# Kernel optimization log

Hardware: AMD Instinct MI355X
Metric: run time of the kernel (lower is better)

The kernel has to match this reference:

```python
import jax, jax.numpy as jnp
import numpy as np

TEMPERATURE = 1.0
NEG = -1e9
EPS = 1e-8


def setup_inputs() -> dict:
    key = jax.random.key(0)
    k1, k2, k3 = jax.random.split(key, 3)
    B, H = 524288, 32
    scores = jax.random.normal(k1, (B, H), dtype=jnp.float32)
    rankings = jax.random.randint(k2, (B, H), 0, 33, dtype=jnp.int32)
    mask = jax.random.randint(k3, (B, H), 0, 2, dtype=jnp.int32).astype(bool)
    return {"scores": scores, "rankings": rankings, "mask": mask}


def reference(scores, rankings, mask):
    B, H = scores.shape
    # effective validity: horse present AND has a ranking > 0 (top_k=None)
    m = mask & (rankings > 0)
    # masked, temperature-scaled scores; -1e9 entries underflow to exactly 0 in softmax
    s = jnp.where(m, scores / TEMPERATURE, NEG)
    p = jax.nn.softmax(s, axis=1)  # [B, H], ~0 at invalid slots

    n_valid = jnp.sum(m, axis=1)  # [B]
    # ideal order: valid horses sorted by ranking ascending (invalid pushed to end)
    rank_key = jnp.where(m, rankings, jnp.iinfo(jnp.int32).max)
    rank_order = jnp.argsort(rank_key, axis=1)          # stable sort
    # prediction order: valid horses in original index order (matches torch.where)
    pos_order = jnp.argsort(~m, axis=1)                 # stable: valid first

    q = jnp.take_along_axis(p, rank_order, axis=1)      # ideal_probs, aligned by list position
    pr = jnp.take_along_axis(p, pos_order, axis=1)      # pred_probs,  aligned by list position

    # positions >= n_valid are padding
    valid_pos = jnp.arange(H)[None, :] < n_valid[:, None]
    q_safe = jnp.where(valid_pos, q, 1.0)
    pr_safe = jnp.where(valid_pos, pr, 1.0)
    # KL(ideal || pred) with the original's log(pred + 1e-8)
    kl_terms = q_safe * (jnp.log(q_safe) - jnp.log(pr_safe + EPS))
    kl = jnp.sum(jnp.where(valid_pos, kl_terms, 0.0), axis=1)  # [B]

    # rows with <= 1 valid ranked horse are skipped entirely
    row_ok = n_valid > 1
    n_rows = jnp.maximum(jnp.sum(row_ok), 1)
    return jnp.sum(jnp.where(row_ok, kl, 0.0)) / n_rows  # reduction='mean'
```

## Files before the change

### kernel.cpp

```cpp
#include <hip/hip_runtime.h>
#include <stdint.h>


typedef short s16x2 __attribute__((ext_vector_type(2)));
union PK { uint32_t u; s16x2 v; };

#define H 32
#define BLK 256

__global__ __launch_bounds__(BLK) void listwise_kernel(
    const float* __restrict__ scores,
    const int* __restrict__ rankings,
    const unsigned char* __restrict__ mask_u8,
    float* __restrict__ part_kl,
    float* __restrict__ part_cnt,
    int nrows)
{
    __shared__ unsigned short lds[BLK * 34];
    __shared__ float s_kl[4], s_cnt[4];

    const int tid  = threadIdx.x;
    const int lane = tid & 63;
    const int wid  = tid >> 6;
    const int row  = blockIdx.x * BLK + tid;

    unsigned char probe = mask_u8[lane];
    const bool mask_is_i32 =
        (__ballot(((lane & 3) != 0) && (probe != 0)) == 0ull);

    float kl = 0.0f, cnt = 0.0f;

    if (row < nrows) {
        uint32_t vbits = 0;
        if (mask_is_i32) {
            const int4* p = (const int4*)((const int*)mask_u8 + (size_t)row * H);
            #pragma unroll
            for (int c = 0; c < 8; ++c) {
                int4 v = p[c];
                vbits |= (v.x != 0 ? 1u : 0u) << (4*c+0);
                vbits |= (v.y != 0 ? 1u : 0u) << (4*c+1);
                vbits |= (v.z != 0 ? 1u : 0u) << (4*c+2);
                vbits |= (v.w != 0 ? 1u : 0u) << (4*c+3);
            }
        } else {
            const uint4* p = (const uint4*)(mask_u8 + (size_t)row * H);
            #pragma unroll
            for (int c = 0; c < 2; ++c) {
                uint4 v = p[c];
                uint32_t w[4] = {v.x, v.y, v.z, v.w};
                #pragma unroll
                for (int q = 0; q < 4; ++q)
                    #pragma unroll
                    for (int b = 0; b < 4; ++b)
                        vbits |= ((((w[q] >> (8*b)) & 0xFFu) != 0u) ? 1u : 0u)
                                 << (16*c + 4*q + b);
            }
        }

        uint32_t kp[16], sp[16];
        int nv = 0, jp = 0;
        unsigned short* rowp = &lds[tid * 34];
        {
            const int4*   rp4 = (const int4*)(rankings + (size_t)row * H);
            const float4* sp4 = (const float4*)(scores + (size_t)row * H);
            #pragma unroll
            for (int c = 0; c < 8; ++c) {
                int4   rv = rp4[c];
                float4 sv = sp4[c];
                int    rr[4] = {rv.x, rv.y, rv.z, rv.w};
                float  ss[4] = {sv.x, sv.y, sv.z, sv.w};
                uint32_t kq[4], bq[4];
                #pragma unroll
                for (int q = 0; q < 4; ++q) {
                    const int k = 4*c + q;
                    const bool valid =
                        (((vbits >> k) & 1u) != 0u) && (rr[q] > 0);
                    kq[q] = valid ? ((((uint32_t)rr[q]) << 5) | (uint32_t)k)
                                  : (0x4000u | (uint32_t)k);
                    nv += valid ? 1 : 0;
                    bq[q] = (__float_as_uint(ss[q]) + 0x8000u) >> 16;
                    rowp[valid ? jp : 32] = (unsigned short)bq[q];
                    jp += valid ? 1 : 0;
                }
                kp[2*c]   = kq[0] | (kq[1] << 16);
                kp[2*c+1] = kq[2] | (kq[3] << 16);
                sp[2*c]   = bq[0] | (bq[1] << 16);
                sp[2*c+1] = bq[2] | (bq[3] << 16);
            }
        }

        float se = 0.0f, num = 0.0f;
        #pragma unroll
        for (int i = 0; i < H; ++i) {
            const uint32_t pw = kp[i / 2];
            const uint32_t k16 = (i & 1) ? (pw >> 16) : (pw & 0xFFFFu);
            PK b; b.u = (k16 << 16) | k16;
            PK acc; acc.u = 0;
            #pragma unroll
            for (int m = 0; m < 16; ++m) {
                PK pm; pm.u = kp[m];
                s16x2 d = pm.v - b.v;
                acc.v = acc.v - (d >> 15);
            }
            const int j = (int)acc.v.x + (int)acc.v.y;
            const float g = __uint_as_float(((uint32_t)rowp[j]) << 16);
            const uint32_t sw = sp[i / 2];
            const float s_i = __uint_as_float((i & 1) ? (sw & 0xFFFF0000u)
                                                      : (sw << 16));
            const bool valid = k16 < 0x4000u;
            float e = __expf(s_i);
            e = valid ? e : 0.0f;
            const float d2 = valid ? (s_i - g) : 0.0f;
            se += e;
            num = __builtin_fmaf(e, d2, num);
        }
        if (nv > 1) { kl = __fdividef(num, se); cnt = 1.0f; }
    }

    #pragma unroll
    for (int m = 32; m >= 1; m >>= 1) {
        kl  += __shfl_xor(kl, m);
        cnt += __shfl_xor(cnt, m);
    }
    if (lane == 0) { s_kl[wid] = kl; s_cnt[wid] = cnt; }
    __syncthreads();
    if (tid == 0) {
        part_kl[blockIdx.x]  = s_kl[0] + s_kl[1] + s_kl[2] + s_kl[3];
        part_cnt[blockIdx.x] = s_cnt[0] + s_cnt[1] + s_cnt[2] + s_cnt[3];
    }
}

__global__ __launch_bounds__(256) void finalize_kernel(
    const float* __restrict__ part_kl,
    const float* __restrict__ part_cnt,
    float* __restrict__ out, int nblk)
{
    float k = 0.0f, c = 0.0f;
    for (int i = threadIdx.x; i < nblk; i += 256) {
        k += part_kl[i];
        c += part_cnt[i];
    }
    #pragma unroll
    for (int m = 32; m >= 1; m >>= 1) {
        k += __shfl_xor(k, m);
        c += __shfl_xor(c, m);
    }
    __shared__ float sk[4], sc[4];
    const int wid = threadIdx.x >> 6;
    if ((threadIdx.x & 63) == 0) { sk[wid] = k; sc[wid] = c; }
    __syncthreads();
    if (threadIdx.x == 0) {
        float K = sk[0] + sk[1] + sk[2] + sk[3];
        float C = sc[0] + sc[1] + sc[2] + sc[3];
        if (C < 1.0f) C = 1.0f;
        out[0] = K / C;
    }
}

extern "C" void kernel_launch(void* const* d_in, const int* in_sizes, int n_in,
                              void* d_out, int out_size, void* d_ws, size_t ws_size,
                              hipStream_t stream) {
    const float* scores = (const float*)d_in[0];
    const int* rankings = (const int*)d_in[1];
    const unsigned char* mask = (const unsigned char*)d_in[2];
    float* out = (float*)d_out;

    const int total = in_sizes[0];
    const int nrows = total / H;
    const int blocks = (nrows + BLK - 1) / BLK;

    float* part_kl  = (float*)d_ws;
    float* part_cnt = (float*)d_ws + blocks;

    listwise_kernel<<<blocks, BLK, 0, stream>>>(
        scores, rankings, mask, part_kl, part_cnt, nrows);

    finalize_kernel<<<1, 256, 0, stream>>>(part_kl, part_cnt, out, blocks);
}
```

Before: 209.9 us.

## Stage row loads through per-wave LDS for coalesced global reads

Each thread used to read its own 128-byte row directly, so consecutive lanes hit addresses 128 bytes apart. Now each wave loads its 64 rows cooperatively with lane-contiguous uint4 loads, transposes them through a padded per-wave LDS region, and each lane then reads its row back from LDS. The same region is reused for the mask, rankings, scores and the compacted bf16 scores, so the phases must be ordered carefully within the wave. The change adds LDS traffic and a scalar fallback path for partial tails.

Result: no change. 207.2 us (-1.3%).

```diff
diff --git a/kernel.cpp b/kernel.cpp
--- a/kernel.cpp
+++ b/kernel.cpp
@@ -2,11 +2,14 @@
 #include <stdint.h>
 
 
+#define H 32
+#define BLK 256
+#define WPB 4
+#define WROW 33
+#define WREGION (64 * WROW)
+
 typedef short s16x2 __attribute__((ext_vector_type(2)));
 union PK { uint32_t u; s16x2 v; };
-
-#define H 32
-#define BLK 256
 
 __global__ __launch_bounds__(BLK) void listwise_kernel(
     const float* __restrict__ scores,
@@ -16,13 +19,14 @@
     float* __restrict__ part_cnt,
     int nrows)
 {
-    __shared__ unsigned short lds[BLK * 34];
-    __shared__ float s_kl[4], s_cnt[4];
+    __shared__ uint32_t stage[WPB * WREGION];
+    __shared__ float s_kl[WPB], s_cnt[WPB];
 
     const int tid  = threadIdx.x;
     const int lane = tid & 63;
     const int wid  = tid >> 6;
-    const int row  = blockIdx.x * BLK + tid;
+    uint32_t* wbuf = &stage[wid * WREGION];
+    const int wrow0 = blockIdx.x * BLK + wid * 64;
 
     unsigned char probe = mask_u8[lane];
     const bool mask_is_i32 =
@@ -30,65 +34,131 @@
 
     float kl = 0.0f, cnt = 0.0f;
 
-    if (row < nrows) {
-        uint32_t vbits = 0;
+    uint32_t kp[16], sp[16], vbits = 0;
+    int nv = 0;
+    bool have_row = false;
+    unsigned short* rowp = (unsigned short*)&wbuf[lane * WROW];
+
+    if (wrow0 + 64 <= nrows) {
+        have_row = true;
         if (mask_is_i32) {
-            const int4* p = (const int4*)((const int*)mask_u8 + (size_t)row * H);
+            const uint4* g4 =
+                (const uint4*)((const uint32_t*)mask_u8 + (size_t)wrow0 * H);
             #pragma unroll
             for (int c = 0; c < 8; ++c) {
-                int4 v = p[c];
-                vbits |= (v.x != 0 ? 1u : 0u) << (4*c+0);
-                vbits |= (v.y != 0 ? 1u : 0u) << (4*c+1);
-                vbits |= (v.z != 0 ? 1u : 0u) << (4*c+2);
-                vbits |= (v.w != 0 ? 1u : 0u) << (4*c+3);
-            }
+                uint4 v = g4[lane + 64 * c];
+                const int L = (lane + 64 * c) << 2;
+                uint32_t* d = &wbuf[(L >> 5) * WROW + (L & 31)];
+                d[0] = v.x; d[1] = v.y; d[2] = v.z; d[3] = v.w;
+            }
+            const uint32_t* rb = &wbuf[lane * WROW];
+            #pragma unroll
+            for (int k = 0; k < H; ++k)
+                vbits |= (rb[k] != 0u ? 1u : 0u) << k;
         } else {
-            const uint4* p = (const uint4*)(mask_u8 + (size_t)row * H);
+            const uint4* g4 = (const uint4*)(mask_u8 + (size_t)wrow0 * H);
             #pragma unroll
             for (int c = 0; c < 2; ++c) {
-                uint4 v = p[c];
-                uint32_t w[4] = {v.x, v.y, v.z, v.w};
-                #pragma unroll
-                for (int q = 0; q < 4; ++q)
-                    #pragma unroll
-                    for (int b = 0; b < 4; ++b)
-                        vbits |= ((((w[q] >> (8*b)) & 0xFFu) != 0u) ? 1u : 0u)
-                                 << (16*c + 4*q + b);
-            }
-        }
-
-        uint32_t kp[16], sp[16];
-        int nv = 0, jp = 0;
-        unsigned short* rowp = &lds[tid * 34];
+                uint4 v = g4[lane + 64 * c];
+                const int L = (lane + 64 * c) << 2;
+                uint32_t* d = &wbuf[(L >> 3) * 9 + (L & 7)];
+                d[0] = v.x; d[1] = v.y; d[2] = v.z; d[3] = v.w;
+            }
+            const uint32_t* rb = &wbuf[lane * 9];
+            #pragma unroll
+            for (int dwi = 0; dwi < 8; ++dwi) {
+                uint32_t w = rb[dwi];
+                uint32_t t2 = w | (w >> 1); t2 |= t2 >> 2; t2 |= t2 >> 4;
+                uint32_t nib = ((t2 & 0x01010101u) * 0x01020408u) >> 24;
+                vbits |= (nib & 0xFu) << (dwi * 4);
+            }
+        }
+
         {
-            const int4*   rp4 = (const int4*)(rankings + (size_t)row * H);
-            const float4* sp4 = (const float4*)(scores + (size_t)row * H);
+            const uint4* g4 = (const uint4*)(rankings + (size_t)wrow0 * H);
             #pragma unroll
             for (int c = 0; c < 8; ++c) {
-                int4   rv = rp4[c];
-                float4 sv = sp4[c];
-                int    rr[4] = {rv.x, rv.y, rv.z, rv.w};
-                float  ss[4] = {sv.x, sv.y, sv.z, sv.w};
-                uint32_t kq[4], bq[4];
-                #pragma unroll
-                for (int q = 0; q < 4; ++q) {
-                    const int k = 4*c + q;
-                    const bool valid =
-                        (((vbits >> k) & 1u) != 0u) && (rr[q] > 0);
-                    kq[q] = valid ? ((((uint32_t)rr[q]) << 5) | (uint32_t)k)
-                                  : (0x4000u | (uint32_t)k);
-                    nv += valid ? 1 : 0;
-                    bq[q] = (__float_as_uint(ss[q]) + 0x8000u) >> 16;
-                    rowp[valid ? jp : 32] = (unsigned short)bq[q];
-                    jp += valid ? 1 : 0;
-                }
-                kp[2*c]   = kq[0] | (kq[1] << 16);
-                kp[2*c+1] = kq[2] | (kq[3] << 16);
-                sp[2*c]   = bq[0] | (bq[1] << 16);
-                sp[2*c+1] = bq[2] | (bq[3] << 16);
-            }
-        }
-
+                uint4 v = g4[lane + 64 * c];
+                const int L = (lane + 64 * c) << 2;
+                uint32_t* d = &wbuf[(L >> 5) * WROW + (L & 31)];
+                d[0] = v.x; d[1] = v.y; d[2] = v.z; d[3] = v.w;
+            }
+            const int* rb = (const int*)&wbuf[lane * WROW];
+            #pragma unroll
+            for (int a = 0; a < 16; ++a) {
+                const int r0 = rb[2 * a], r1 = rb[2 * a + 1];
+                const bool v0 = (((vbits >> (2 * a)) & 1u) != 0u) && (r0 > 0);
+                const bool v1 = (((vbits >> (2 * a + 1)) & 1u) != 0u) && (r1 > 0);
+                const uint32_t k0 = v0 ? ((((uint32_t)r0) << 5) | (uint32_t)(2 * a))
+                                       : (0x4000u | (uint32_t)(2 * a));
+                const uint32_t k1 = v1 ? ((((uint32_t)r1) << 5) | (uint32_t)(2 * a + 1))
+                                       : (0x4000u | (uint32_t)(2 * a + 1));
+                kp[a] = k0 | (k1 << 16);
+                nv += (v0 ? 1 : 0) + (v1 ? 1 : 0);
+            }
+        }
+
+        {
+            const uint4* g4 = (const uint4*)(scores + (size_t)wrow0 * H);
+            #pragma unroll
+            for (int c = 0; c < 8; ++c) {
+                uint4 v = g4[lane + 64 * c];
+                const int L = (lane + 64 * c) << 2;
+                uint32_t* d = &wbuf[(L >> 5) * WROW + (L & 31)];
+                d[0] = v.x; d[1] = v.y; d[2] = v.z; d[3] = v.w;
+            }
+            const uint32_t* rb = &wbuf[lane * WROW];
+            int jp = 0;
+            #pragma unroll
+            for (int a = 0; a < 16; ++a) {
+                const uint32_t b0 = (rb[2 * a]     + 0x8000u) >> 16;
+                const uint32_t b1 = (rb[2 * a + 1] + 0x8000u) >> 16;
+                sp[a] = b0 | (b1 << 16);
+                const uint32_t kw = kp[a];
+                const bool v0 = (kw & 0xFFFFu) < 0x4000u;
+                const bool v1 = (kw >> 16) < 0x4000u;
+                rowp[v0 ? jp : 64] = (unsigned short)b0;
+                jp += v0 ? 1 : 0;
+                rowp[v1 ? jp : 64] = (unsigned short)b1;
+                jp += v1 ? 1 : 0;
+            }
+        }
+    } else if (wrow0 + lane < nrows) {
+        have_row = true;
+        const int row = wrow0 + lane;
+        const int*   rptr = rankings + (size_t)row * H;
+        const float* sptr = scores + (size_t)row * H;
+        if (mask_is_i32) {
+            const int* mp = (const int*)mask_u8 + (size_t)row * H;
+            #pragma unroll
+            for (int k = 0; k < H; ++k) vbits |= (mp[k] != 0 ? 1u : 0u) << k;
+        } else {
+            const unsigned char* mp = mask_u8 + (size_t)row * H;
+            #pragma unroll
+            for (int k = 0; k < H; ++k) vbits |= (mp[k] != 0 ? 1u : 0u) << k;
+        }
+        int jp = 0;
+        #pragma unroll
+        for (int a = 0; a < 16; ++a) {
+            uint32_t kq[2], bq[2];
+            #pragma unroll
+            for (int q = 0; q < 2; ++q) {
+                const int k = 2 * a + q;
+                const int r = rptr[k];
+                const bool valid = (((vbits >> k) & 1u) != 0u) && (r > 0);
+                kq[q] = valid ? ((((uint32_t)r) << 5) | (uint32_t)k)
+                              : (0x4000u | (uint32_t)k);
+                nv += valid ? 1 : 0;
+                bq[q] = (__float_as_uint(sptr[k]) + 0x8000u) >> 16;
+                rowp[valid ? jp : 64] = (unsigned short)bq[q];
+                jp += valid ? 1 : 0;
+            }
+            kp[a] = kq[0] | (kq[1] << 16);
+            sp[a] = bq[0] | (bq[1] << 16);
+        }
+    }
+
+    if (have_row) {
         float se = 0.0f, num = 0.0f;
         #pragma unroll
         for (int i = 0; i < H; ++i) {
```
